# Optimization experiments

Hardware: AMD Instinct MI355X
Metric: run time of the kernel (lower is better)

## Reference

```python
import jax, jax.numpy as jnp
import numpy as np

N_REP = 8      # N: repeated gelu(LN(linear)) blocks
M_LAYERS = 4   # M: transformer encoder layers
SEQ = 100
D = 4
FF = 2048      # PyTorch TransformerEncoderLayer default dim_feedforward
H = 4          # nhead; head_dim = 1


def _ln(x, g, b, axes):
    m = jnp.mean(x, axis=axes, keepdims=True)
    v = jnp.var(x, axis=axes, keepdims=True)
    return (x - m) / jnp.sqrt(v + 1e-5) * g + b


def _encoder_layer(x, Win, bi, Wout, bout, W1, b1, W2, b2, g1, be1, g2, be2):
    # x: [S, Nb, D] with S = batch_size (batch_first=False!), Nb = 100
    S, Nb, E = x.shape
    qkv = x @ Win.T + bi                      # [S, Nb, 3D]
    q, k, v = jnp.split(qkv, 3, axis=-1)
    qh = q.reshape(S, Nb, H, E // H)          # head_dim = 1, scale 1/sqrt(1)=1
    kh = k.reshape(S, Nb, H, E // H)
    vh = v.reshape(S, Nb, H, E // H)
    scores = jnp.einsum('snhd,tnhd->nhst', qh, kh)   # [Nb, H, S, S]
    attn = jax.nn.softmax(scores, axis=-1)
    o = jnp.einsum('nhst,tnhd->snhd', attn, vh).reshape(S, Nb, E)
    o = o @ Wout.T + bout
    x = _ln(x + o, g1, be1, (-1,))            # post-norm (norm_first=False)
    f = jax.nn.relu(x @ W1.T + b1) @ W2.T + b2
    return _ln(x + f, g2, be2, (-1,))


def setup_inputs() -> dict:
    key = jax.random.key(0)
    ks = jax.random.split(key, 24)
    B = 256
    d = {}
    d['x'] = jax.random.normal(ks[0], (B, SEQ, D), dtype=jnp.float32)
    # conv1: kernel_size=1, 1->1 channel -> scalar affine
    d['conv_w'] = jax.random.normal(ks[1], (), dtype=jnp.float32) * 0.5 + 1.0
    d['conv_b'] = jax.random.normal(ks[2], (), dtype=jnp.float32) * 0.1
    # shared 4x4 linear (self.liner) and LayerNorm([100,4])
    d['Wl'] = jax.random.normal(ks[3], (D, D), dtype=jnp.float32) * 0.5
    d['bl'] = jax.random.normal(ks[4], (D,), dtype=jnp.float32) * 0.1
    d['ln_g'] = jnp.ones((SEQ, D), dtype=jnp.float32)
    d['ln_b'] = jnp.zeros((SEQ, D), dtype=jnp.float32)
    # transformer encoder params, stacked over M layers
    s = 0.3
    d['Win'] = jax.random.normal(ks[5], (M_LAYERS, 3 * D, D), dtype=jnp.float32) * s
    d['bi'] = jax.random.normal(ks[6], (M_LAYERS, 3 * D), dtype=jnp.float32) * 0.05
    d['Wout'] = jax.random.normal(ks[7], (M_LAYERS, D, D), dtype=jnp.float32) * s
    d['bout'] = jax.random.normal(ks[8], (M_LAYERS, D), dtype=jnp.float32) * 0.05
    d['W1'] = jax.random.normal(ks[9], (M_LAYERS, FF, D), dtype=jnp.float32) * 0.05
    d['b1'] = jax.random.normal(ks[10], (M_LAYERS, FF), dtype=jnp.float32) * 0.05
    d['W2'] = jax.random.normal(ks[11], (M_LAYERS, D, FF), dtype=jnp.float32) * 0.02
    d['b2'] = jax.random.normal(ks[12], (M_LAYERS, D), dtype=jnp.float32) * 0.05
    d['g1'] = jnp.ones((M_LAYERS, D), dtype=jnp.float32)
    d['be1'] = jnp.zeros((M_LAYERS, D), dtype=jnp.float32)
    d['g2'] = jnp.ones((M_LAYERS, D), dtype=jnp.float32)
    d['be2'] = jnp.zeros((M_LAYERS, D), dtype=jnp.float32)
    return d


def reference(x, conv_w, conv_b, Wl, bl, ln_g, ln_b,
              Win, bi, Wout, bout, W1, b1, W2, b2, g1, be1, g2, be2):
    # per-channel kernel_size=1 conv == elementwise affine (same scalar for all 4 channels)
    h = x * conv_w + conv_b                   # [B, 100, 4]
    for _ in range(N_REP):
        h = jax.nn.gelu(_ln(h @ Wl.T + bl, ln_g, ln_b, (-2, -1)), approximate=False)
    h = h @ Wl.T + bl
    for i in range(M_LAYERS):
        h = _encoder_layer(h, Win[i], bi[i], Wout[i], bout[i], W1[i], b1[i],
                           W2[i], b2[i], g1[i], be1[i], g2[i], be2[i])
    h = h @ Wl.T + bl
    return jax.nn.softmax(h, axis=2)
```

## Files before the change

kernel.cpp:

```cpp
#include <hip/hip_runtime.h>
#include <math.h>

#define SEQ   100
#define BATCH 256
#define NREP  8
#define FFD   2048
#define RSQRT2 0.70710678118654752440f

typedef __attribute__((ext_vector_type(16))) float fv16;
typedef __attribute__((ext_vector_type(4)))  float fv4;

__device__ __forceinline__ float wsum(float v) {
#pragma unroll
  for (int o = 32; o > 0; o >>= 1) v += __shfl_xor(v, o, 64);
  return v;
}

__global__ __launch_bounds__(256) void k_prepA(
    const float* __restrict__ W1, const float* __restrict__ b1,
    const float* __restrict__ W2, float* __restrict__ Wp,
    const float* __restrict__ x, const float* __restrict__ convw,
    const float* __restrict__ convb, const float* __restrict__ Wl,
    const float* __restrict__ bl, const float* __restrict__ lng,
    const float* __restrict__ lnb, float* __restrict__ XT)
{
  const int t = threadIdx.x;
  if (blockIdx.x < 8) {
    const int id = blockIdx.x * 256 + t;
    const int l = id >> 9, g = id & 511, f0 = g * 4;
    float* dst = Wp + id * 36;
    const float* w1 = W1 + (l * FFD + f0) * 4;
#pragma unroll
    for (int i = 0; i < 16; ++i) dst[i] = w1[i];
    const float* w2 = W2 + l * 4 * FFD;
#pragma unroll
    for (int f = 0; f < 4; ++f)
#pragma unroll
      for (int d = 0; d < 4; ++d) dst[16 + f * 4 + d] = w2[d * FFD + f0 + f];
    const float* bb = b1 + l * FFD + f0;
#pragma unroll
    for (int f = 0; f < 4; ++f) dst[32 + f] = bb[f];
    return;
  }

  const int b = (blockIdx.x - 8) * 4 + (t >> 6);
  const int lane = t & 63;
  const bool act = lane < 50;

  const float cw = convw[0], cb = convb[0];
  float W[4][4], B[4];
#pragma unroll
  for (int j = 0; j < 4; ++j) {
    B[j] = bl[j];
#pragma unroll
    for (int d = 0; d < 4; ++d) W[j][d] = Wl[j * 4 + d];
  }
  float h[2][4] = {{0.f,0.f,0.f,0.f},{0.f,0.f,0.f,0.f}};
  float gg[2][4] = {{0.f}}, eb[2][4] = {{0.f}};
  if (act) {
#pragma unroll
    for (int p = 0; p < 2; ++p) {
      const int r = lane * 2 + p;
      float4 xr = *(const float4*)(x + (b * SEQ + r) * 4);
      h[p][0] = fmaf(xr.x, cw, cb); h[p][1] = fmaf(xr.y, cw, cb);
      h[p][2] = fmaf(xr.z, cw, cb); h[p][3] = fmaf(xr.w, cw, cb);
      float4 gv = *(const float4*)(lng + r * 4);
      float4 bv = *(const float4*)(lnb + r * 4);
      gg[p][0] = gv.x; gg[p][1] = gv.y; gg[p][2] = gv.z; gg[p][3] = gv.w;
      eb[p][0] = bv.x; eb[p][1] = bv.y; eb[p][2] = bv.z; eb[p][3] = bv.w;
    }
  }
  for (int it = 0; it < NREP; ++it) {
    float y[2][4] = {{0.f,0.f,0.f,0.f},{0.f,0.f,0.f,0.f}};
    float s1 = 0.f, s2 = 0.f;
    if (act) {
#pragma unroll
      for (int p = 0; p < 2; ++p)
#pragma unroll
        for (int j = 0; j < 4; ++j) {
          float yy = B[j];
#pragma unroll
          for (int d = 0; d < 4; ++d) yy = fmaf(h[p][d], W[j][d], yy);
          y[p][j] = yy; s1 += yy; s2 = fmaf(yy, yy, s2);
        }
    }
    s1 = wsum(s1); s2 = wsum(s2);
    const float mean = s1 * (1.0f / 400.0f);
    const float var  = s2 * (1.0f / 400.0f) - mean * mean;
    const float rstd = rsqrtf(var + 1e-5f);
    if (act) {
#pragma unroll
      for (int p = 0; p < 2; ++p)
#pragma unroll
        for (int j = 0; j < 4; ++j) {
          float vv = fmaf((y[p][j] - mean) * rstd, gg[p][j], eb[p][j]);
          h[p][j] = 0.5f * vv * (1.0f + erff(vv * RSQRT2));
        }
    }
  }
  if (act) {
#pragma unroll
    for (int p = 0; p < 2; ++p) {
      const int r = lane * 2 + p;
      float yy[4];
#pragma unroll
      for (int j = 0; j < 4; ++j) {
        float a = B[j];
#pragma unroll
        for (int d = 0; d < 4; ++d) a = fmaf(h[p][d], W[j][d], a);
        yy[j] = a;
      }
      *(float4*)(XT + (r * BATCH + b) * 4) =
          make_float4(yy[0], yy[1], yy[2], yy[3]);
    }
  }
}

__global__ __launch_bounds__(512, 4) void k_layer(
    const float* __restrict__ XTin, float* __restrict__ XTout,
    const float* __restrict__ Wa,  const float* __restrict__ ba,
    const float* __restrict__ Wo,  const float* __restrict__ bo,
    const float* __restrict__ Wpl, const float* __restrict__ b2l,
    const float* __restrict__ g1l, const float* __restrict__ e1l,
    const float* __restrict__ g2l, const float* __restrict__ e2l,
    const float* __restrict__ Wl,  const float* __restrict__ bl,
    float* __restrict__ out, const int last)
{
  const int n     = blockIdx.x;
  const int qbase = blockIdx.y * 64;
  const int t     = threadIdx.x;
  const int lane  = t & 63;
  const int wv    = t >> 6;
  const int ah    = wv & 3;
  const int kh    = wv >> 2;

  __shared__ __align__(16) float2 kv[4][256];
  __shared__ float2 part[4][64][3];
  __shared__ float  osm[4][64];
  __shared__ float  x1s[64][4];
  __shared__ float  pacc[8][64][4];
  __shared__ float2 kred[4][2];

  {
    const int s = t & 255, hp = t >> 8;
    float4 xr = *(const float4*)(XTin + (n * BATCH + s) * 4);
#pragma unroll
    for (int i = 0; i < 2; ++i) {
      const int hh = hp * 2 + i;
      const float* wk = Wa + (4 + hh) * 4;
      const float* wp = Wa + (8 + hh) * 4;
      float k = ba[4+hh] + xr.x*wk[0] + xr.y*wk[1] + xr.z*wk[2] + xr.w*wk[3];
      float v = ba[8+hh] + xr.x*wp[0] + xr.y*wp[1] + xr.z*wp[2] + xr.w*wp[3];
      kv[hh][s] = make_float2(k, v);
    }
  }
  float q;
  {
    const float* wq = Wa + ah * 4;
    float4 xa = *(const float4*)(XTin + (n * BATCH + qbase + lane) * 4);
    q = ba[ah] + xa.x*wq[0] + xa.y*wq[1] + xa.z*wq[2] + xa.w*wq[3];
  }
  __syncthreads();

  {
    float a = kv[ah][kh * 128 + lane].x;
    float c = kv[ah][kh * 128 + 64 + lane].x;
    float mx = fmaxf(a, c), mn = fminf(a, c);
#pragma unroll
    for (int o = 32; o > 0; o >>= 1) {
      mx = fmaxf(mx, __shfl_xor(mx, o, 64));
      mn = fminf(mn, __shfl_xor(mn, o, 64));
    }
    if (lane == 0) kred[ah][kh] = make_float2(mx, mn);
  }
  __syncthreads();

  {
    const float kmx = fmaxf(kred[ah][0].x, kred[ah][1].x);
    const float kmn = fminf(kred[ah][0].y, kred[ah][1].y);
    const float m = (q >= 0.f) ? q * kmx : q * kmn;
    float d0 = 0.f, d1 = 0.f, n0 = 0.f, n1 = 0.f;
#pragma unroll
    for (int w = 0; w < 2; ++w) {
      const int kb = kh * 128 + w * 64;
#pragma unroll 4
      for (int i = 0; i < 32; ++i) {
        const int p = ((lane + i) & 31) * 2;
        float4 kk = *(const float4*)&kv[ah][kb + p];
        float p0 = __expf(fmaf(q, kk.x, -m));
        float p1 = __expf(fmaf(q, kk.z, -m));
        d0 += p0; n0 = fmaf(p0, kk.y, n0);
        d1 += p1; n1 = fmaf(p1, kk.w, n1);
      }
    }
    part[ah][lane][kh] = make_float2(d0 + d1, n0 + n1);
  }
  __syncthreads();

  if (t < 256) {
    const int h = t >> 6, r = t & 63;
    float2 a = part[h][r][0], b = part[h][r][1];
    osm[h][r] = (a.y + b.y) / (a.x + b.x);
  }
  __syncthreads();

  if (t < 256) {
    const int r = t >> 2, d = t & 3;
    const float o0 = osm[0][r], o1 = osm[1][r], o2 = osm[2][r], o3 = osm[3][r];
    float rr = XTin[(n * BATCH + qbase + r) * 4 + d] + bo[d]
             + o0*Wo[d*4+0] + o1*Wo[d*4+1] + o2*Wo[d*4+2] + o3*Wo[d*4+3];
    float sum = rr + __shfl_xor(rr, 1, 64); sum += __shfl_xor(sum, 2, 64);
    const float mean = 0.25f * sum;
    const float dv = rr - mean;
    float qq = dv * dv;
    float qs = qq + __shfl_xor(qq, 1, 64); qs += __shfl_xor(qs, 2, 64);
    const float rstd = rsqrtf(0.25f * qs + 1e-5f);
    x1s[r][d] = fmaf(dv * rstd, g1l[d], e1l[d]);
  }
  __syncthreads();

  {
    const int wvu = __builtin_amdgcn_readfirstlane(wv);
    const float* gp = Wpl + (size_t)wvu * 2304;
    const float x0 = x1s[lane][0], x1 = x1s[lane][1];
    const float x2 = x1s[lane][2], x3 = x1s[lane][3];
    float a0 = 0.f, a1 = 0.f, a2 = 0.f, a3 = 0.f;
#pragma unroll
    for (int g = 0; g < 64; ++g) {
      fv16 w1, w2; fv4 bb;
      asm("s_load_dwordx16 %0, %3, %4\n\t"
          "s_load_dwordx16 %1, %3, %5\n\t"
          "s_load_dwordx4  %2, %3, %6\n\t"
          "s_waitcnt lgkmcnt(0)"
          : "=s"(w1), "=s"(w2), "=s"(bb)
          : "s"(gp), "i"(144 * g), "i"(144 * g + 64), "i"(144 * g + 128));
#pragma unroll
      for (int f = 0; f < 4; ++f) {
        const float w10 = w1[f*4+0], w11 = w1[f*4+1];
        const float w12 = w1[f*4+2], w13 = w1[f*4+3];
        const float w20 = w2[f*4+0], w21 = w2[f*4+1];
        const float w22 = w2[f*4+2], w23 = w2[f*4+3];
        float hh = fmaf(x3, w13, fmaf(x2, w12, fmaf(x1, w11, fmaf(x0, w10, bb[f]))));
        hh = fmaxf(hh, 0.f);
        a0 = fmaf(hh, w20, a0); a1 = fmaf(hh, w21, a1);
        a2 = fmaf(hh, w22, a2); a3 = fmaf(hh, w23, a3);
      }
    }
    *(float4*)&pacc[wv][lane][0] = make_float4(a0, a1, a2, a3);
  }
  __syncthreads();

  if (t < 256) {
    const int r = t >> 2, d = t & 3;
    float s8 = b2l[d];
#pragma unroll
    for (int w = 0; w < 8; ++w) s8 += pacc[w][r][d];
    float val = x1s[r][d] + s8;
    float sum = val + __shfl_xor(val, 1, 64); sum += __shfl_xor(sum, 2, 64);
    const float mean = 0.25f * sum;
    const float dv = val - mean;
    float qq = dv * dv;
    float qs = qq + __shfl_xor(qq, 1, 64); qs += __shfl_xor(qs, 2, 64);
    const float rstd = rsqrtf(0.25f * qs + 1e-5f);
    const float res = fmaf(dv * rstd, g2l[d], e2l[d]);
    if (!last) XTout[(n * BATCH + qbase + r) * 4 + d] = res;
    else       x1s[r][d] = res;
  }

  if (last) {
    __syncthreads();
    if (t < 256) {
      const int r = t >> 2, j = t & 3;
      const float y = fmaf(x1s[r][3], Wl[j*4+3], fmaf(x1s[r][2], Wl[j*4+2],
                      fmaf(x1s[r][1], Wl[j*4+1], fmaf(x1s[r][0], Wl[j*4+0], bl[j]))));
      float mx = fmaxf(y, __shfl_xor(y, 1, 64)); mx = fmaxf(mx, __shfl_xor(mx, 2, 64));
      const float e = __expf(y - mx);
      float se = e + __shfl_xor(e, 1, 64); se += __shfl_xor(se, 2, 64);
      out[((qbase + r) * SEQ + n) * 4 + j] = e / se;
    }
  }
}

extern "C" void kernel_launch(void* const* d_in, const int* in_sizes, int n_in,
                              void* d_out, int out_size, void* d_ws, size_t ws_size,
                              hipStream_t stream)
{
  const float* x     = (const float*)d_in[0];
  const float* convw = (const float*)d_in[1];
  const float* convb = (const float*)d_in[2];
  const float* Wl    = (const float*)d_in[3];
  const float* bl    = (const float*)d_in[4];
  const float* lng   = (const float*)d_in[5];
  const float* lnb   = (const float*)d_in[6];
  const float* Win   = (const float*)d_in[7];
  const float* bi    = (const float*)d_in[8];
  const float* Wout  = (const float*)d_in[9];
  const float* bout  = (const float*)d_in[10];
  const float* W1    = (const float*)d_in[11];
  const float* b1    = (const float*)d_in[12];
  const float* W2    = (const float*)d_in[13];
  const float* b2    = (const float*)d_in[14];
  const float* g1    = (const float*)d_in[15];
  const float* be1   = (const float*)d_in[16];
  const float* g2    = (const float*)d_in[17];
  const float* be2   = (const float*)d_in[18];

  float* XT0 = (float*)d_ws;
  float* XT1 = XT0 + SEQ * BATCH * 4;
  float* Wp  = XT1 + SEQ * BATCH * 4;

  k_prepA<<<72, 256, 0, stream>>>(W1, b1, W2, Wp,
                                  x, convw, convb, Wl, bl, lng, lnb, XT0);
  for (int l = 0; l < 4; ++l) {
    const float* in  = (l & 1) ? XT1 : XT0;
    float*       outb= (l & 1) ? XT0 : XT1;
    k_layer<<<dim3(SEQ, 4), 512, 0, stream>>>(
        in, outb,
        Win + l * 48, bi + l * 12, Wout + l * 16, bout + l * 4,
        Wp + l * 512 * 36, b2 + l * 4,
        g1 + l * 4, be1 + l * 4, g2 + l * 4, be2 + l * 4,
        Wl, bl, (float*)d_out, (l == 3) ? 1 : 0);
  }
}
```

Measured before the change: 133.9 us.

## Fuse four encoder layer launches into one persistent per-sequence kernel

Replaces the four per-layer launches with one kernel. Each 1024-thread block keeps all 256 rows for one sequence position in shared memory and runs all four layers plus the final projection and softmax. This removes three launches and the global round-trips of activations between layers. Each wave now handles four rows per thread in the FFN so the scalar-loaded weights are reused more. The cost is a grid of only 100 blocks, which leaves many of the GPU's compute units idle where the old grid had 400 blocks per layer.

```diff
diff --git a/kernel.cpp b/kernel.cpp
--- a/kernel.cpp
+++ b/kernel.cpp
@@ -116,168 +116,198 @@
   }
 }
 
-__global__ __launch_bounds__(512, 4) void k_layer(
-    const float* __restrict__ XTin, float* __restrict__ XTout,
-    const float* __restrict__ Wa,  const float* __restrict__ ba,
-    const float* __restrict__ Wo,  const float* __restrict__ bo,
-    const float* __restrict__ Wpl, const float* __restrict__ b2l,
-    const float* __restrict__ g1l, const float* __restrict__ e1l,
-    const float* __restrict__ g2l, const float* __restrict__ e2l,
+__global__ __launch_bounds__(1024, 4) void k_encoder(
+    const float* __restrict__ XT,
+    const float* __restrict__ Win, const float* __restrict__ bi,
+    const float* __restrict__ Wout, const float* __restrict__ bout,
+    const float* __restrict__ Wp,  const float* __restrict__ b2,
+    const float* __restrict__ g1,  const float* __restrict__ be1,
+    const float* __restrict__ g2,  const float* __restrict__ be2,
     const float* __restrict__ Wl,  const float* __restrict__ bl,
-    float* __restrict__ out, const int last)
+    float* __restrict__ out)
 {
-  const int n     = blockIdx.x;
-  const int qbase = blockIdx.y * 64;
-  const int t     = threadIdx.x;
-  const int lane  = t & 63;
-  const int wv    = t >> 6;
-  const int ah    = wv & 3;
-  const int kh    = wv >> 2;
-
-  __shared__ __align__(16) float2 kv[4][256];
-  __shared__ float2 part[4][64][3];
-  __shared__ float  osm[4][64];
-  __shared__ float  x1s[64][4];
-  __shared__ float  pacc[8][64][4];
-  __shared__ float2 kred[4][2];
-
-  {
-    const int s = t & 255, hp = t >> 8;
-    float4 xr = *(const float4*)(XTin + (n * BATCH + s) * 4);
-#pragma unroll
-    for (int i = 0; i < 2; ++i) {
-      const int hh = hp * 2 + i;
+  const int n    = blockIdx.x;
+  const int t    = threadIdx.x;
+  const int lane = t & 63;
+  const int wv   = t >> 6;
+
+  __shared__ float  xs[256][4];
+  __shared__ float2 kv[4][256];
+  __shared__ float  osm[4][256];
+  __shared__ float  x1s[256][4];
+  __shared__ float4 pacc[8][256];
+  __shared__ float2 kred[4][4];
+
+  if (t < 256) {
+    float4 v = *(const float4*)(XT + (n * BATCH + t) * 4);
+    xs[t][0] = v.x; xs[t][1] = v.y; xs[t][2] = v.z; xs[t][3] = v.w;
+  }
+  __syncthreads();
+
+  for (int l = 0; l < 4; ++l) {
+    const float* Wa  = Win + l * 48;
+    const float* ba  = bi + l * 12;
+    const float* Wo  = Wout + l * 16;
+    const float* bo  = bout + l * 4;
+    const float* Wpl = Wp + l * 512 * 36;
+    const float* b2l = b2 + l * 4;
+    const float* g1l = g1 + l * 4;  const float* e1l = be1 + l * 4;
+    const float* g2l = g2 + l * 4;  const float* e2l = be2 + l * 4;
+
+    {
+      const int s = t & 255, hh = t >> 8;
+      const float x0 = xs[s][0], x1 = xs[s][1], x2 = xs[s][2], x3 = xs[s][3];
       const float* wk = Wa + (4 + hh) * 4;
       const float* wp = Wa + (8 + hh) * 4;
-      float k = ba[4+hh] + xr.x*wk[0] + xr.y*wk[1] + xr.z*wk[2] + xr.w*wk[3];
-      float v = ba[8+hh] + xr.x*wp[0] + xr.y*wp[1] + xr.z*wp[2] + xr.w*wp[3];
+      float k = ba[4+hh] + x0*wk[0] + x1*wk[1] + x2*wk[2] + x3*wk[3];
+      float v = ba[8+hh] + x0*wp[0] + x1*wp[1] + x2*wp[2] + x3*wp[3];
       kv[hh][s] = make_float2(k, v);
     }
-  }
-  float q;
+    __syncthreads();
+
+    {
+      const int h = wv & 3, strip = wv >> 2;
+      float k = kv[h][strip * 64 + lane].x;
+      float mx = k, mn = k;
+#pragma unroll
+      for (int o = 32; o > 0; o >>= 1) {
+        mx = fmaxf(mx, __shfl_xor(mx, o, 64));
+        mn = fminf(mn, __shfl_xor(mn, o, 64));
+      }
+      if (lane == 0) kred[h][strip] = make_float2(mx, mn);
+    }
+    __syncthreads();
+
+    if (t < 512) {
+      const int h = t >> 7, rp = t & 127;
+      const int r0 = 2 * rp, r1 = 2 * rp + 1;
+      const float* wq = Wa + h * 4;
+      const float q0 = ba[h] + xs[r0][0]*wq[0] + xs[r0][1]*wq[1]
+                             + xs[r0][2]*wq[2] + xs[r0][3]*wq[3];
+      const float q1 = ba[h] + xs[r1][0]*wq[0] + xs[r1][1]*wq[1]
+                             + xs[r1][2]*wq[2] + xs[r1][3]*wq[3];
+      const float kmx = fmaxf(fmaxf(kred[h][0].x, kred[h][1].x),
+                              fmaxf(kred[h][2].x, kred[h][3].x));
+      const float kmn = fminf(fminf(kred[h][0].y, kred[h][1].y),
+                              fminf(kred[h][2].y, kred[h][3].y));
+      const float m0 = (q0 >= 0.f) ? q0 * kmx : q0 * kmn;
+      const float m1 = (q1 >= 0.f) ? q1 * kmx : q1 * kmn;
+      float dA = 0.f, nA = 0.f, dB = 0.f, nB = 0.f;
+#pragma unroll 4
+      for (int i = 0; i < 128; ++i) {
+        const int p = (i + 2 * lane) & 127;
+        float4 kk = *(const float4*)&kv[h][p * 2];
+        float pA0 = __expf(fmaf(q0, kk.x, -m0));
+        float pA1 = __expf(fmaf(q0, kk.z, -m0));
+        float pB0 = __expf(fmaf(q1, kk.x, -m1));
+        float pB1 = __expf(fmaf(q1, kk.z, -m1));
+        dA += pA0 + pA1; nA = fmaf(pA1, kk.w, fmaf(pA0, kk.y, nA));
+        dB += pB0 + pB1; nB = fmaf(pB1, kk.w, fmaf(pB0, kk.y, nB));
+      }
+      osm[h][r0] = nA / dA;
+      osm[h][r1] = nB / dB;
+    }
+    __syncthreads();
+
+    {
+      const int r = t >> 2, d = t & 3;
+      const float o0 = osm[0][r], o1 = osm[1][r], o2 = osm[2][r], o3 = osm[3][r];
+      float rr = xs[r][d] + bo[d] + o0*Wo[d*4+0] + o1*Wo[d*4+1]
+                                  + o2*Wo[d*4+2] + o3*Wo[d*4+3];
+      float sum = rr + __shfl_xor(rr, 1, 64); sum += __shfl_xor(sum, 2, 64);
+      const float mean = 0.25f * sum;
+      const float dv = rr - mean;
+      float qq = dv * dv;
+      float qs = qq + __shfl_xor(qq, 1, 64); qs += __shfl_xor(qs, 2, 64);
+      const float rstd = rsqrtf(0.25f * qs + 1e-5f);
+      x1s[r][d] = fmaf(dv * rstd, g1l[d], e1l[d]);
+    }
+    __syncthreads();
+
+    float acc[4][4] = {{0.f,0.f,0.f,0.f},{0.f,0.f,0.f,0.f},
+                       {0.f,0.f,0.f,0.f},{0.f,0.f,0.f,0.f}};
+    {
+      const int wvu = __builtin_amdgcn_readfirstlane(wv);
+      const float* gp = Wpl + (size_t)wvu * 1152;
+      float xr[4][4];
+#pragma unroll
+      for (int k = 0; k < 4; ++k) {
+        const int r = k * 64 + lane;
+        xr[k][0] = x1s[r][0]; xr[k][1] = x1s[r][1];
+        xr[k][2] = x1s[r][2]; xr[k][3] = x1s[r][3];
+      }
+#pragma unroll
+      for (int g = 0; g < 32; ++g) {
+        fv16 w1v, w2v; fv4 bbv;
+        asm("s_load_dwordx16 %0, %3, %4\n\t"
+            "s_load_dwordx16 %1, %3, %5\n\t"
+            "s_load_dwordx4  %2, %3, %6\n\t"
+            "s_waitcnt lgkmcnt(0)"
+            : "=s"(w1v), "=s"(w2v), "=s"(bbv)
+            : "s"(gp), "i"(144 * g), "i"(144 * g + 64), "i"(144 * g + 128));
+#pragma unroll
+        for (int f = 0; f < 4; ++f) {
+          const float w10 = w1v[f*4+0], w11 = w1v[f*4+1];
+          const float w12 = w1v[f*4+2], w13 = w1v[f*4+3];
+          const float w20 = w2v[f*4+0], w21 = w2v[f*4+1];
+          const float w22 = w2v[f*4+2], w23 = w2v[f*4+3];
+          const float bf  = bbv[f];
+#pragma unroll
+          for (int k = 0; k < 4; ++k) {
+            float hh = fmaf(xr[k][3], w13, fmaf(xr[k][2], w12,
+                       fmaf(xr[k][1], w11, fmaf(xr[k][0], w10, bf))));
+            hh = fmaxf(hh, 0.f);
+            acc[k][0] = fmaf(hh, w20, acc[k][0]);
+            acc[k][1] = fmaf(hh, w21, acc[k][1]);
+            acc[k][2] = fmaf(hh, w22, acc[k][2]);
+            acc[k][3] = fmaf(hh, w23, acc[k][3]);
+          }
+        }
+      }
+    }
+    if (wv < 8) {
+#pragma unroll
+      for (int k = 0; k < 4; ++k)
+        pacc[wv][k * 64 + lane] =
+            make_float4(acc[k][0], acc[k][1], acc[k][2], acc[k][3]);
+    }
+    __syncthreads();
+    if (wv >= 8) {
+#pragma unroll
+      for (int k = 0; k < 4; ++k) {
+        float4 o = pacc[wv - 8][k * 64 + lane];
+        o.x += acc[k][0]; o.y += acc[k][1];
+        o.z += acc[k][2]; o.w += acc[k][3];
+        pacc[wv - 8][k * 64 + lane] = o;
+      }
+    }
+    __syncthreads();
+
+    {
+      const int r = t >> 2, d = t & 3;
+      float s8 = b2l[d];
+#pragma unroll
+      for (int w = 0; w < 8; ++w) s8 += ((const float*)&pacc[w][r])[d];
+      float val = x1s[r][d] + s8;
+      float sum = val + __shfl_xor(val, 1, 64); sum += __shfl_xor(sum, 2, 64);
+      const float mean = 0.25f * sum;
+      const float dv = val - mean;
+      float qq = dv * dv;
+      float qs = qq + __shfl_xor(qq, 1, 64); qs += __shfl_xor(qs, 2, 64);
+      const float rstd = rsqrtf(0.25f * qs + 1e-5f);
+      xs[r][d] = fmaf(dv * rstd, g2l[d], e2l[d]);
+    }
+    __syncthreads();
+  }
+
   {
-    const float* wq = Wa + ah * 4;
-    float4 xa = *(const float4*)(XTin + (n * BATCH + qbase + lane) * 4);
-    q = ba[ah] + xa.x*wq[0] + xa.y*wq[1] + xa.z*wq[2] + xa.w*wq[3];
-  }
-  __syncthreads();
-
-  {
-    float a = kv[ah][kh * 128 + lane].x;
-    float c = kv[ah][kh * 128 + 64 + lane].x;
-    float mx = fmaxf(a, c), mn = fminf(a, c);
-#pragma unroll
-    for (int o = 32; o > 0; o >>= 1) {
-      mx = fmaxf(mx, __shfl_xor(mx, o, 64));
-      mn = fminf(mn, __shfl_xor(mn, o, 64));
-    }
-    if (lane == 0) kred[ah][kh] = make_float2(mx, mn);
-  }
-  __syncthreads();
-
-  {
-    const float kmx = fmaxf(kred[ah][0].x, kred[ah][1].x);
-    const float kmn = fminf(kred[ah][0].y, kred[ah][1].y);
-    const float m = (q >= 0.f) ? q * kmx : q * kmn;
-    float d0 = 0.f, d1 = 0.f, n0 = 0.f, n1 = 0.f;
-#pragma unroll
-    for (int w = 0; w < 2; ++w) {
-      const int kb = kh * 128 + w * 64;
-#pragma unroll 4
-      for (int i = 0; i < 32; ++i) {
-        const int p = ((lane + i) & 31) * 2;
-        float4 kk = *(const float4*)&kv[ah][kb + p];
-        float p0 = __expf(fmaf(q, kk.x, -m));
-        float p1 = __expf(fmaf(q, kk.z, -m));
-        d0 += p0; n0 = fmaf(p0, kk.y, n0);
-        d1 += p1; n1 = fmaf(p1, kk.w, n1);
-      }
-    }
-    part[ah][lane][kh] = make_float2(d0 + d1, n0 + n1);
-  }
-  __syncthreads();
-
-  if (t < 256) {
-    const int h = t >> 6, r = t & 63;
-    float2 a = part[h][r][0], b = part[h][r][1];
-    osm[h][r] = (a.y + b.y) / (a.x + b.x);
-  }
-  __syncthreads();
-
-  if (t < 256) {
-    const int r = t >> 2, d = t & 3;
-    const float o0 = osm[0][r], o1 = osm[1][r], o2 = osm[2][r], o3 = osm[3][r];
-    float rr = XTin[(n * BATCH + qbase + r) * 4 + d] + bo[d]
-             + o0*Wo[d*4+0] + o1*Wo[d*4+1] + o2*Wo[d*4+2] + o3*Wo[d*4+3];
-    float sum = rr + __shfl_xor(rr, 1, 64); sum += __shfl_xor(sum, 2, 64);
-    const float mean = 0.25f * sum;
-    const float dv = rr - mean;
-    float qq = dv * dv;
-    float qs = qq + __shfl_xor(qq, 1, 64); qs += __shfl_xor(qs, 2, 64);
-    const float rstd = rsqrtf(0.25f * qs + 1e-5f);
-    x1s[r][d] = fmaf(dv * rstd, g1l[d], e1l[d]);
-  }
-  __syncthreads();
-
-  {
-    const int wvu = __builtin_amdgcn_readfirstlane(wv);
-    const float* gp = Wpl + (size_t)wvu * 2304;
-    const float x0 = x1s[lane][0], x1 = x1s[lane][1];
-    const float x2 = x1s[lane][2], x3 = x1s[lane][3];
-    float a0 = 0.f, a1 = 0.f, a2 = 0.f, a3 = 0.f;
-#pragma unroll
-    for (int g = 0; g < 64; ++g) {
-      fv16 w1, w2; fv4 bb;
-      asm("s_load_dwordx16 %0, %3, %4\n\t"
-          "s_load_dwordx16 %1, %3, %5\n\t"
-          "s_load_dwordx4  %2, %3, %6\n\t"
-          "s_waitcnt lgkmcnt(0)"
-          : "=s"(w1), "=s"(w2), "=s"(bb)
-          : "s"(gp), "i"(144 * g), "i"(144 * g + 64), "i"(144 * g + 128));
-#pragma unroll
-      for (int f = 0; f < 4; ++f) {
-        const float w10 = w1[f*4+0], w11 = w1[f*4+1];
-        const float w12 = w1[f*4+2], w13 = w1[f*4+3];
-        const float w20 = w2[f*4+0], w21 = w2[f*4+1];
-        const float w22 = w2[f*4+2], w23 = w2[f*4+3];
-        float hh = fmaf(x3, w13, fmaf(x2, w12, fmaf(x1, w11, fmaf(x0, w10, bb[f]))));
-        hh = fmaxf(hh, 0.f);
-        a0 = fmaf(hh, w20, a0); a1 = fmaf(hh, w21, a1);
-        a2 = fmaf(hh, w22, a2); a3 = fmaf(hh, w23, a3);
-      }
-    }
-    *(float4*)&pacc[wv][lane][0] = make_float4(a0, a1, a2, a3);
-  }
-  __syncthreads();
-
-  if (t < 256) {
-    const int r = t >> 2, d = t & 3;
-    float s8 = b2l[d];
-#pragma unroll
-    for (int w = 0; w < 8; ++w) s8 += pacc[w][r][d];
-    float val = x1s[r][d] + s8;
-    float sum = val + __shfl_xor(val, 1, 64); sum += __shfl_xor(sum, 2, 64);
-    const float mean = 0.25f * sum;
-    const float dv = val - mean;
-    float qq = dv * dv;
-    float qs = qq + __shfl_xor(qq, 1, 64); qs += __shfl_xor(qs, 2, 64);
-    const float rstd = rsqrtf(0.25f * qs + 1e-5f);
-    const float res = fmaf(dv * rstd, g2l[d], e2l[d]);
-    if (!last) XTout[(n * BATCH + qbase + r) * 4 + d] = res;
-    else       x1s[r][d] = res;
-  }
-
-  if (last) {
-    __syncthreads();
-    if (t < 256) {
-      const int r = t >> 2, j = t & 3;
-      const float y = fmaf(x1s[r][3], Wl[j*4+3], fmaf(x1s[r][2], Wl[j*4+2],
-                      fmaf(x1s[r][1], Wl[j*4+1], fmaf(x1s[r][0], Wl[j*4+0], bl[j]))));
-      float mx = fmaxf(y, __shfl_xor(y, 1, 64)); mx = fmaxf(mx, __shfl_xor(mx, 2, 64));
-      const float e = __expf(y - mx);
-      float se = e + __shfl_xor(e, 1, 64); se += __shfl_xor(se, 2, 64);
-      out[((qbase + r) * SEQ + n) * 4 + j] = e / se;
-    }
+    const int r = t >> 2, j = t & 3;
+    const float y = fmaf(xs[r][3], Wl[j*4+3], fmaf(xs[r][2], Wl[j*4+2],
+                    fmaf(xs[r][1], Wl[j*4+1], fmaf(xs[r][0], Wl[j*4+0], bl[j]))));
+    float mx = fmaxf(y, __shfl_xor(y, 1, 64)); mx = fmaxf(mx, __shfl_xor(mx, 2, 64));
+    const float e = __expf(y - mx);
+    float se = e + __shfl_xor(e, 1, 64); se += __shfl_xor(se, 2, 64);
+    out[(r * SEQ + n) * 4 + j] = e / se;
   }
 }
 
@@ -305,20 +335,12 @@
   const float* g2    = (const float*)d_in[17];
   const float* be2   = (const float*)d_in[18];
 
-  float* XT0 = (float*)d_ws;
-  float* XT1 = XT0 + SEQ * BATCH * 4;
-  float* Wp  = XT1 + SEQ * BATCH * 4;
+  float* XT = (float*)d_ws;
+  float* Wp = XT + SEQ * BATCH * 4;
 
   k_prepA<<<72, 256, 0, stream>>>(W1, b1, W2, Wp,
-                                  x, convw, convb, Wl, bl, lng, lnb, XT0);
-  for (int l = 0; l < 4; ++l) {
-    const float* in  = (l & 1) ? XT1 : XT0;
-    float*       outb= (l & 1) ? XT0 : XT1;
-    k_layer<<<dim3(SEQ, 4), 512, 0, stream>>>(
-        in, outb,
-        Win + l * 48, bi + l * 12, Wout + l * 16, bout + l * 4,
-        Wp + l * 512 * 36, b2 + l * 4,
-        g1 + l * 4, be1 + l * 4, g2 + l * 4, be2 + l * 4,
-        Wl, bl, (float*)d_out, (l == 3) ? 1 : 0);
-  }
+                                  x, convw, convb, Wl, bl, lng, lnb, XT);
+  k_encoder<<<SEQ, 1024, 0, stream>>>(XT, Win, bi, Wout, bout, Wp, b2,
+                                      g1, be1, g2, be2, Wl, bl,
+                                      (float*)d_out);
 }
```

Result: slower. 193.9 us (+44.9%).
